# Optimization experiments

Measured on AMD Instinct MI355X. Metric: run time of the kernel, lower is better.

Reference implementation:

```python
import jax, jax.numpy as jnp
import numpy as np

B, N, D_IN, D_OUT = 4, 2048, 1024, 1024

def setup_inputs() -> dict:
    key = jax.random.key(0)
    ks = jax.random.split(key, 7)
    s_in = 1.0 / np.sqrt(D_IN)
    return {
        "X": jax.random.normal(ks[0], (B, N, D_IN), dtype=jnp.float32),
        "Wq": jax.random.uniform(ks[1], (D_IN, D_OUT), jnp.float32, -s_in, s_in),
        "bq": jax.random.uniform(ks[2], (D_OUT,), jnp.float32, -s_in, s_in),
        "Wk": jax.random.uniform(ks[3], (D_IN, D_OUT), jnp.float32, -s_in, s_in),
        "bk": jax.random.uniform(ks[4], (D_OUT,), jnp.float32, -s_in, s_in),
        "Wv": jax.random.uniform(ks[5], (D_IN, D_OUT), jnp.float32, -s_in, s_in),
        "bv": jax.random.uniform(ks[6], (D_OUT,), jnp.float32, -s_in, s_in),
    }

def reference(X, Wq, bq, Wk, bk, Wv, bv):
    # QKV projections: [B,N,D_in] @ [D_in,D_out] -> [B,N,D_out]
    q = jnp.einsum('bnd,de->bne', X, Wq) + bq
    k = jnp.einsum('bnd,de->bne', X, Wk) + bk
    v = jnp.einsum('bnd,de->bne', X, Wv) + bv
    # Unscaled attention (faithful: original has no 1/sqrt(d))
    scores = jnp.einsum('bne,bme->bnm', q, k)  # [B,N,N]
    weights = jax.nn.softmax(scores, axis=-1)
    return jnp.einsum('bnm,bme->bne', weights, v)
```

## Files before the change

kernel.cpp:

```cpp
#include <hip/hip_runtime.h>
#include <hip/hip_bf16.h>
#include <hip/hip_fp16.h>
#include <stdint.h>
#include <math.h>


typedef unsigned short ushort_t;
typedef __attribute__((ext_vector_type(8))) _Float16  f16x8;
typedef __attribute__((ext_vector_type(4))) _Float16  f16x4;
typedef __attribute__((ext_vector_type(4))) float     f32x4;

__device__ __forceinline__ void async_load16(const void* g, void* l) {
  __builtin_amdgcn_global_load_lds(
      (const __attribute__((address_space(1))) void*)g,
      (__attribute__((address_space(3))) void*)l, 16, 0, 0);
}

#define BARR do { __builtin_amdgcn_sched_barrier(0); \
                  __builtin_amdgcn_s_barrier();      \
                  __builtin_amdgcn_sched_barrier(0); } while (0)

#define A0OFF 0
#define B0OFF 16384
#define A1OFF 32768
#define B1OFF 49152

template<int SHIFT>
__device__ __forceinline__ void stage_half(const ushort_t* __restrict__ gb,
                                           int k0, int q, ushort_t* lt, int t)
{
#pragma unroll
  for (int j = 0; j < 2; ++j) {
    const int i   = j * 64 + (t >> 3);
    const int row = ((i >> SHIFT) << (SHIFT + 1)) | (q << SHIFT) | (i & ((1 << SHIFT) - 1));
    const int ch  = (t & 7) ^ (row & 7);
    async_load16(gb + (long)row * 1024 + k0 + ch * 8, lt + row * 64 + (t & 7) * 8);
  }
}

#define RD_A(TP, QM)                                                          \
  do { _Pragma("unroll") for (int m_ = 0; m_ < 4; ++m_) {                     \
    af[m_][0] = *(const f16x8*)&(TP)[(arow0 + (QM)*64 + m_*16) * 64 + ck0];   \
    af[m_][1] = *(const f16x8*)&(TP)[(arow0 + (QM)*64 + m_*16) * 64 + ck1];   \
  } } while (0)

#define RD_B(TP, QN)                                                          \
  do { _Pragma("unroll") for (int n_ = 0; n_ < 2; ++n_) {                     \
    bf[n_][0] = *(const f16x8*)&(TP)[(brow0 + (QN)*32 + n_*16) * 64 + ck0];   \
    bf[n_][1] = *(const f16x8*)&(TP)[(brow0 + (QN)*32 + n_*16) * 64 + ck1];   \
  } } while (0)

#define MM(QM, QN)                                                            \
  do { __builtin_amdgcn_s_setprio(1);                                         \
  _Pragma("unroll") for (int kh_ = 0; kh_ < 2; ++kh_)                         \
    _Pragma("unroll") for (int m_ = 0; m_ < 4; ++m_)                          \
      _Pragma("unroll") for (int n_ = 0; n_ < 2; ++n_)                        \
        acc[(QM)*4+m_][(QN)*2+n_] = __builtin_amdgcn_mfma_f32_16x16x32_f16(   \
            af[m_][kh_], bf[n_][kh_], acc[(QM)*4+m_][(QN)*2+n_], 0, 0, 0);    \
  __builtin_amdgcn_s_setprio(0); } while (0)

template<bool LAST>
__device__ __forceinline__ void iter256(const ushort_t* __restrict__ Ab,
                                        const ushort_t* __restrict__ Bb,
                                        ushort_t* lds, f32x4 (&acc)[8][4],
                                        int ka, int t, int arow0, int brow0,
                                        int ck0, int ck1)
{
  const int kb = ka + 64, kc = ka + 128, kd = ka + 192;
  f16x8 af[4][2], bf[2][2];

  RD_A(lds + A0OFF, 0); RD_B(lds + B0OFF, 0);
  stage_half<5>(Bb, kb, 0, lds + B1OFF, t);
  BARR; MM(0, 0); BARR;

  RD_B(lds + B0OFF, 1);
  if constexpr (!LAST) stage_half<6>(Ab, kc, 0, lds + A0OFF, t);
  BARR; MM(0, 1); BARR;

  RD_A(lds + A0OFF, 1);
  if constexpr (!LAST) stage_half<5>(Bb, kc, 1, lds + B0OFF, t);
  BARR; MM(1, 1); BARR;

  RD_B(lds + B0OFF, 0);
  if constexpr (!LAST) stage_half<6>(Ab, kc, 1, lds + A0OFF, t);
  BARR; MM(1, 0);
  if constexpr (LAST) asm volatile("s_waitcnt vmcnt(0)" ::: "memory");
  else                asm volatile("s_waitcnt vmcnt(6)" ::: "memory");
  BARR;

  RD_A(lds + A1OFF, 0); RD_B(lds + B1OFF, 0);
  if constexpr (!LAST) stage_half<5>(Bb, kc, 0, lds + B0OFF, t);
  BARR; MM(0, 0); BARR;

  RD_B(lds + B1OFF, 1);
  if constexpr (!LAST) stage_half<6>(Ab, kd, 0, lds + A1OFF, t);
  BARR; MM(0, 1); BARR;

  RD_A(lds + A1OFF, 1);
  if constexpr (!LAST) stage_half<5>(Bb, kd, 1, lds + B1OFF, t);
  BARR; MM(1, 1); BARR;

  RD_B(lds + B1OFF, 0);
  if constexpr (!LAST) stage_half<6>(Ab, kd, 1, lds + A1OFF, t);
  BARR; MM(1, 0);
  if constexpr (!LAST) asm volatile("s_waitcnt vmcnt(6)" ::: "memory");
  BARR;
}

__device__ __forceinline__ void gemm256(const ushort_t* __restrict__ Ab,
                                        const ushort_t* __restrict__ Bb,
                                        ushort_t* lds, f32x4 (&acc)[8][4])
{
  const int t    = threadIdx.x;
  const int lane = t & 63;
  const int wave = t >> 6;
  const int wr   = wave >> 2;
  const int wc   = wave & 3;
  const int arow0 = wr * 128 + (lane & 15);
  const int brow0 = wc * 64  + (lane & 15);
  const int ck0 = (((lane >> 4)    ) ^ (lane & 7)) * 8;
  const int ck1 = ((4 + (lane >> 4)) ^ (lane & 7)) * 8;

  stage_half<6>(Ab,  0, 0, lds + A0OFF, t);
  stage_half<5>(Bb,  0, 1, lds + B0OFF, t);
  stage_half<6>(Ab,  0, 1, lds + A0OFF, t);
  stage_half<5>(Bb,  0, 0, lds + B0OFF, t);
  stage_half<6>(Ab, 64, 0, lds + A1OFF, t);
  stage_half<5>(Bb, 64, 1, lds + B1OFF, t);
  stage_half<6>(Ab, 64, 1, lds + A1OFF, t);
  asm volatile("s_waitcnt vmcnt(6)" ::: "memory");
  BARR;

#pragma unroll 1
  for (int it = 0; it < 7; ++it)
    iter256<false>(Ab, Bb, lds, acc, it * 128, t, arow0, brow0, ck0, ck1);
  iter256<true>(Ab, Bb, lds, acc, 896, t, arow0, brow0, ck0, ck1);
}

#define NA0 0
#define NB0 16384
#define NA1 24576
#define NB1 40960

__device__ __forceinline__ void stage_A_n(const ushort_t* __restrict__ gb, long ldk,
                                          int k0, int q, ushort_t* lt, int t)
{
#pragma unroll
  for (int j = 0; j < 2; ++j) {
    const int i   = j * 64 + (t >> 3);
    const int row = ((i >> 5) << 6) | (q << 5) | (i & 31);
    const int ch  = (t & 7) ^ (row & 7);
    async_load16(gb + (long)row * ldk + k0 + ch * 8, lt + row * 64 + (t & 7) * 8);
  }
}

__device__ __forceinline__ void stage_B_n(const ushort_t* __restrict__ gb, long ldk,
                                          int k0, int q, ushort_t* lt, int t)
{
  const int i   = t >> 3;
  const int row = ((i >> 5) << 6) | (q << 5) | (i & 31);
  const int ch  = (t & 7) ^ (row & 7);
  async_load16(gb + (long)row * ldk + k0 + ch * 8, lt + row * 64 + (t & 7) * 8);
}

#define RDN_A(TP, QM)                                                         \
  do { _Pragma("unroll") for (int m_ = 0; m_ < 2; ++m_) {                     \
    af[m_][0] = *(const f16x8*)&(TP)[(arow_l + (QM)*32 + m_*16) * 64 + ck0];  \
    af[m_][1] = *(const f16x8*)&(TP)[(arow_l + (QM)*32 + m_*16) * 64 + ck1];  \
  } } while (0)

#define RDN_AS(TP, QM, S)                                                     \
  do { _Pragma("unroll") for (int m_ = 0; m_ < 2; ++m_) {                     \
    af[m_][0] = *(const f16x8*)&(TP)[(arow_l + (QM)*32 + m_*16) * 64 + ck0] * (S)[(QM)*2+m_]; \
    af[m_][1] = *(const f16x8*)&(TP)[(arow_l + (QM)*32 + m_*16) * 64 + ck1] * (S)[(QM)*2+m_]; \
  } } while (0)

#define RDN_B2(TP, QN, BF)                                                    \
  do { _Pragma("unroll") for (int n_ = 0; n_ < 2; ++n_) {                     \
    (BF)[n_][0] = *(const f16x8*)&(TP)[(brow_l + (QN)*32 + n_*16) * 64 + ck0];\
    (BF)[n_][1] = *(const f16x8*)&(TP)[(brow_l + (QN)*32 + n_*16) * 64 + ck1];\
  } } while (0)

#define MM2(QM)                                                               \
  do { __builtin_amdgcn_s_setprio(1);                                         \
  _Pragma("unroll") for (int kh_ = 0; kh_ < 2; ++kh_)                         \
    _Pragma("unroll") for (int m_ = 0; m_ < 2; ++m_)                          \
      _Pragma("unroll") for (int n_ = 0; n_ < 2; ++n_) {                      \
        acc[(QM)*2+m_][n_]   = __builtin_amdgcn_mfma_f32_16x16x32_f16(        \
            af[m_][kh_], bq0[n_][kh_], acc[(QM)*2+m_][n_], 0, 0, 0);          \
        acc[(QM)*2+m_][2+n_] = __builtin_amdgcn_mfma_f32_16x16x32_f16(        \
            af[m_][kh_], bq1[n_][kh_], acc[(QM)*2+m_][2+n_], 0, 0, 0);        \
      }                                                                       \
  __builtin_amdgcn_s_setprio(0); } while (0)

template<bool LAST>
__device__ __forceinline__ void iter4_n(const ushort_t* __restrict__ Ab,
                                        const ushort_t* __restrict__ Bb,
                                        long lda, long ldb,
                                        ushort_t* lds, f32x4 (&acc)[4][4],
                                        int ka, int t, int arow_l, int brow_l,
                                        int ck0, int ck1)
{
  const int kb = ka + 64, kc = ka + 128, kd = ka + 192;
  f16x8 af[2][2], bq0[2][2], bq1[2][2];

  RDN_A(lds + NA0, 0);
  RDN_B2(lds + NB0, 0, bq0);
  RDN_B2(lds + NB0, 1, bq1);
  stage_B_n(Bb, ldb, kb, 1, lds + NB1, t);
  stage_A_n(Ab, lda, kb, 1, lds + NA1, t);
  BARR; MM2(0); BARR;

  RDN_A(lds + NA0, 1);
  if constexpr (!LAST) {
    stage_A_n(Ab, lda, kc, 0, lds + NA0, t);
    stage_B_n(Bb, ldb, kc, 0, lds + NB0, t);
  }
  BARR; MM2(1);
  if constexpr (LAST) asm volatile("s_waitcnt vmcnt(0)" ::: "memory");
  else                asm volatile("s_waitcnt vmcnt(3)" ::: "memory");
  BARR;

  RDN_A(lds + NA1, 0);
  RDN_B2(lds + NB1, 0, bq0);
  RDN_B2(lds + NB1, 1, bq1);
  if constexpr (!LAST) {
    stage_B_n(Bb, ldb, kc, 1, lds + NB0, t);
    stage_A_n(Ab, lda, kc, 1, lds + NA0, t);
  }
  BARR; MM2(0); BARR;

  RDN_A(lds + NA1, 1);
  if constexpr (!LAST) {
    stage_A_n(Ab, lda, kd, 0, lds + NA1, t);
    stage_B_n(Bb, ldb, kd, 0, lds + NB1, t);
  }
  BARR; MM2(1);
  if constexpr (!LAST) asm volatile("s_waitcnt vmcnt(3)" ::: "memory");
  BARR;
}

template<bool LAST>
__device__ __forceinline__ void pv_iter4(const ushort_t* __restrict__ Ab,
                                         const ushort_t* __restrict__ Bb,
                                         ushort_t* lds, const float (*ScL)[256],
                                         f32x4 (&acc)[4][4],
                                         int ka, int t, int arow_l, int brow_l,
                                         int ck0, int ck1)
{
  const int kb = ka + 64, kc = ka + 128, kd = ka + 192;
  const int cba = ka >> 6;
  f16x8 af[2][2], bq0[2][2], bq1[2][2];
  _Float16 sa[4], sb[4];
#pragma unroll
  for (int s = 0; s < 4; ++s) {
    sa[s] = (_Float16)ScL[cba][arow_l + s * 16];
    sb[s] = (_Float16)ScL[cba + 1][arow_l + s * 16];
  }

  RDN_AS(lds + NA0, 0, sa);
  RDN_B2(lds + NB0, 0, bq0);
  RDN_B2(lds + NB0, 1, bq1);
  stage_B_n(Bb, 2048, kb, 1, lds + NB1, t);
  stage_A_n(Ab, 2048, kb, 1, lds + NA1, t);
  BARR; MM2(0); BARR;

  RDN_AS(lds + NA0, 1, sa);
  if constexpr (!LAST) {
    stage_A_n(Ab, 2048, kc, 0, lds + NA0, t);
    stage_B_n(Bb, 2048, kc, 0, lds + NB0, t);
  }
  BARR; MM2(1);
  if constexpr (LAST) asm volatile("s_waitcnt vmcnt(0)" ::: "memory");
  else                asm volatile("s_waitcnt vmcnt(3)" ::: "memory");
  BARR;

  RDN_AS(lds + NA1, 0, sb);
  RDN_B2(lds + NB1, 0, bq0);
  RDN_B2(lds + NB1, 1, bq1);
  if constexpr (!LAST) {
    stage_B_n(Bb, 2048, kc, 1, lds + NB0, t);
    stage_A_n(Ab, 2048, kc, 1, lds + NA0, t);
  }
  BARR; MM2(0); BARR;

  RDN_AS(lds + NA1, 1, sb);
  if constexpr (!LAST) {
    stage_A_n(Ab, 2048, kd, 0, lds + NA1, t);
    stage_B_n(Bb, 2048, kd, 0, lds + NB1, t);
  }
  BARR; MM2(1);
  if constexpr (!LAST) asm volatile("s_waitcnt vmcnt(3)" ::: "memory");
  BARR;
}

#define PROLOGUE4(LDA, LDB)                                 \
  do {                                                      \
    stage_A_n(Ab, (LDA),  0, 0, lds + NA0, t);              \
    stage_B_n(Bb, (LDB),  0, 0, lds + NB0, t);              \
    stage_B_n(Bb, (LDB),  0, 1, lds + NB0, t);              \
    stage_A_n(Ab, (LDA),  0, 1, lds + NA0, t);              \
    stage_A_n(Ab, (LDA), 64, 0, lds + NA1, t);              \
    stage_B_n(Bb, (LDB), 64, 0, lds + NB1, t);              \
    asm volatile("s_waitcnt vmcnt(3)" ::: "memory");        \
    BARR;                                                   \
  } while (0)

__global__ __launch_bounds__(512, 2)
void qkv4_kernel(const ushort_t* __restrict__ A, const ushort_t* __restrict__ BT,
                 const float* __restrict__ bq, const float* __restrict__ bk,
                 const float* __restrict__ bvp,
                 __half* __restrict__ Qh, __half* __restrict__ Kh,
                 ushort_t* __restrict__ Vt)
{
  __shared__ __align__(16) ushort_t lds[49152];

  const int nb = gridDim.x * gridDim.y;
  int id = blockIdx.y * gridDim.x + blockIdx.x;
  id = (id & 7) * (nb >> 3) + (id >> 3);
  const int bx = id % gridDim.x;
  const int by = id / gridDim.x;

  const ushort_t* Ab = A  + (long)by * 256 * 1024;
  const ushort_t* Bb = BT + (long)bx * 128 * 1024;

  const int t    = threadIdx.x;
  const int lane = t & 63;
  const int wave = t >> 6;
  const int wr   = wave >> 1;
  const int wc   = wave & 1;
  const int arow_l = wr * 64 + (lane & 15);
  const int brow_l = wc * 64 + (lane & 15);
  const int ck0 = (((lane >> 4)    ) ^ (lane & 7)) * 8;
  const int ck1 = ((4 + (lane >> 4)) ^ (lane & 7)) * 8;

  f32x4 acc[4][4];
  const f32x4 zero = {0.0f, 0.0f, 0.0f, 0.0f};
#pragma unroll
  for (int i = 0; i < 4; ++i)
#pragma unroll
    for (int j = 0; j < 4; ++j) acc[i][j] = zero;

  PROLOGUE4(1024, 1024);
#pragma unroll 1
  for (int it = 0; it < 7; ++it)
    iter4_n<false>(Ab, Bb, 1024, 1024, lds, acc, it * 128, t, arow_l, brow_l, ck0, ck1);
  iter4_n<true>(Ab, Bb, 1024, 1024, lds, acc, 896, t, arow_l, brow_l, ck0, ck1);

  const int er = (lane >> 4) * 4, ec = lane & 15;
  const int tgt = bx >> 3;
  const float* bias = (tgt == 0) ? bq : (tgt == 1) ? bk : bvp;

#pragma unroll
  for (int ni = 0; ni < 4; ++ni) {
    const int col = (bx & 7) * 128 + wc * 64 + ni * 16 + ec;
    const float bval = bias[col];
#pragma unroll
    for (int mi = 0; mi < 4; ++mi) {
      const long grow0 = (long)by * 256 + wr * 64 + mi * 16 + er;
      if (tgt < 2) {
        __half* o = (tgt == 0) ? Qh : Kh;
#pragma unroll
        for (int r = 0; r < 4; ++r)
          o[(grow0 + r) * 1024 + col] = __float2half(acc[mi][ni][r] + bval);
      } else {
        const long b  = grow0 >> 11;
        const long ml = grow0 & 2047;
        f16x4 v4;
#pragma unroll
        for (int r = 0; r < 4; ++r) v4[r] = (_Float16)(acc[mi][ni][r] + bval);
        *(f16x4*)&Vt[b * 2097152 + (long)col * 2048 + ml] = v4;
      }
    }
  }
}

__global__ __launch_bounds__(512, 2)
void qk256_kernel(const ushort_t* __restrict__ Q, const ushort_t* __restrict__ Kh,
                  __half* __restrict__ S, float* __restrict__ PM, float* __restrict__ PS)
{
  __shared__ __align__(16) ushort_t lds[65536];

  const int nb = gridDim.x * gridDim.y;
  int id = blockIdx.y * gridDim.x + blockIdx.x;
  id = (id & 7) * (nb >> 3) + (id >> 3);
  const int bx = id % gridDim.x;
  const int by = id / gridDim.x;
  const long z = blockIdx.z;

  const ushort_t* Ab = Q  + z * 2048 * 1024 + (long)by * 256 * 1024;
  const ushort_t* Bb = Kh + z * 2048 * 1024 + (long)bx * 256 * 1024;
  __half* Sb = S + z * 2048 * 2048;

  f32x4 acc[8][4];
  const f32x4 zero = {0.0f, 0.0f, 0.0f, 0.0f};
#pragma unroll
  for (int i = 0; i < 8; ++i)
#pragma unroll
    for (int j = 0; j < 4; ++j) acc[i][j] = zero;

  gemm256(Ab, Bb, lds, acc);

  const int t = threadIdx.x, lane = t & 63, wave = t >> 6;
  const int wr = wave >> 2, wc = wave & 3;
  const int er = (lane >> 4) * 4, ec = lane & 15;
  const int cc = bx * 4 + wc;
  float* PMb = PM + z * 32 * 2048 + (long)cc * 2048;
  float* PSb = PS + z * 32 * 2048 + (long)cc * 2048;

#pragma unroll
  for (int m8 = 0; m8 < 8; ++m8)
#pragma unroll
    for (int r = 0; r < 4; ++r) {
      float m = fmaxf(fmaxf(acc[m8][0][r], acc[m8][1][r]),
                      fmaxf(acc[m8][2][r], acc[m8][3][r]));
      m = fmaxf(m, __shfl_xor(m, 1));
      m = fmaxf(m, __shfl_xor(m, 2));
      m = fmaxf(m, __shfl_xor(m, 4));
      m = fmaxf(m, __shfl_xor(m, 8));
      float s = 0.0f;
#pragma unroll
      for (int n4 = 0; n4 < 4; ++n4) {
        const float e = __expf(acc[m8][n4][r] - m);
        acc[m8][n4][r] = e;
        s += e;
      }
      s += __shfl_xor(s, 1);
      s += __shfl_xor(s, 2);
      s += __shfl_xor(s, 4);
      s += __shfl_xor(s, 8);
      if (ec == 0) {
        const long row = (long)by * 256 + wr * 128 + m8 * 16 + er + r;
        PMb[row] = m;
        PSb[row] = s;
      }
    }

#pragma unroll
  for (int n4 = 0; n4 < 4; ++n4) {
    const long col = (long)bx * 256 + wc * 64 + n4 * 16 + ec;
#pragma unroll
    for (int m8 = 0; m8 < 8; ++m8)
#pragma unroll
      for (int r = 0; r < 4; ++r) {
        const long grow = (long)by * 256 + wr * 128 + m8 * 16 + er + r;
        Sb[grow * 2048 + col] = __float2half(acc[m8][n4][r]);
      }
  }
}

__global__ __launch_bounds__(512, 2)
void pv4_kernel(const ushort_t* __restrict__ S, const ushort_t* __restrict__ Vt,
                const float* __restrict__ PM, const float* __restrict__ PS,
                float* __restrict__ Out)
{
  __shared__ __align__(16) ushort_t lds[49152];
  __shared__ float ScL[32][256];

  const int nb = gridDim.x * gridDim.y;
  int id = blockIdx.y * gridDim.x + blockIdx.x;
  id = (id & 7) * (nb >> 3) + (id >> 3);
  const int bx = id % gridDim.x;
  const int by = id / gridDim.x;
  const long z = blockIdx.z;

  const ushort_t* Ab = S  + z * 4194304 + (long)by * 256 * 2048;
  const ushort_t* Bb = Vt + z * 2097152 + (long)bx * 128 * 2048;
  float* Cb = Out + z * 2048 * 1024;

  const int t = threadIdx.x;

  if (t < 256) {
    const long row = (long)by * 256 + t;
    const float* PMb = PM + z * 32 * 2048;
    const float* PSb = PS + z * 32 * 2048;
    float pm[32];
    float m = -3.4e38f;
#pragma unroll
    for (int cb = 0; cb < 32; ++cb) {
      pm[cb] = PMb[(long)cb * 2048 + row];
      m = fmaxf(m, pm[cb]);
    }
    float l = 0.0f;
#pragma unroll
    for (int cb = 0; cb < 32; ++cb)
      l += PSb[(long)cb * 2048 + row] * __expf(pm[cb] - m);
    const float inv = 1.0f / l;
#pragma unroll
    for (int cb = 0; cb < 32; ++cb)
      ScL[cb][t] = __expf(pm[cb] - m) * inv;
  }
  __syncthreads();

  const int lane = t & 63;
  const int wave = t >> 6;
  const int wr   = wave >> 1;
  const int wc   = wave & 1;
  const int arow_l = wr * 64 + (lane & 15);
  const int brow_l = wc * 64 + (lane & 15);
  const int ck0 = (((lane >> 4)    ) ^ (lane & 7)) * 8;
  const int ck1 = ((4 + (lane >> 4)) ^ (lane & 7)) * 8;

  f32x4 acc[4][4];
  const f32x4 zero = {0.0f, 0.0f, 0.0f, 0.0f};
#pragma unroll
  for (int i = 0; i < 4; ++i)
#pragma unroll
    for (int j = 0; j < 4; ++j) acc[i][j] = zero;

  PROLOGUE4(2048, 2048);
#pragma unroll 1
  for (int it = 0; it < 15; ++it)
    pv_iter4<false>(Ab, Bb, lds, ScL, acc, it * 128, t, arow_l, brow_l, ck0, ck1);
  pv_iter4<true>(Ab, Bb, lds, ScL, acc, 1920, t, arow_l, brow_l, ck0, ck1);

  const int er = (lane >> 4) * 4, ec = lane & 15;
#pragma unroll
  for (int ni = 0; ni < 4; ++ni) {
    const int gcol = bx * 128 + wc * 64 + ni * 16 + ec;
#pragma unroll
    for (int mi = 0; mi < 4; ++mi) {
#pragma unroll
      for (int r = 0; r < 4; ++r) {
        const long grow = (long)by * 256 + wr * 64 + mi * 16 + er + r;
        Cb[grow * 1024 + gcol] = acc[mi][ni][r];
      }
    }
  }
}

__global__ __launch_bounds__(256)
void prep_kernel(const float* __restrict__ W0, const float* __restrict__ W1,
                 const float* __restrict__ W2, __half* __restrict__ dstW,
                 const float* __restrict__ X, __half* __restrict__ Xh)
{
  __shared__ float tile[32][33];
  const int z = blockIdx.z;
  if (z < 3) {
    const float* src = (z == 0) ? W0 : (z == 1) ? W1 : W2;
    __half* d = dstW + (long)z * 1024 * 1024;
    const int c0 = blockIdx.x * 32;
    const int r0 = blockIdx.y * 32;
    const int tx = threadIdx.x & 31;
    const int ty = threadIdx.x >> 5;
#pragma unroll
    for (int i = 0; i < 32; i += 8)
      tile[ty + i][tx] = src[(long)(r0 + ty + i) * 1024 + (c0 + tx)];
    __syncthreads();
#pragma unroll
    for (int i = 0; i < 32; i += 8)
      d[(long)(c0 + ty + i) * 1024 + (r0 + tx)] = __float2half(tile[tx][ty + i]);
  } else {
    const int bid = blockIdx.y * gridDim.x + blockIdx.x;
    const long i = (((long)(z - 3) * 1024 + bid) * 256 + threadIdx.x) * 8;
    const float4 a = *(const float4*)(X + i);
    const float4 b = *(const float4*)(X + i + 4);
    f16x8 h;
    h[0] = (_Float16)a.x; h[1] = (_Float16)a.y; h[2] = (_Float16)a.z; h[3] = (_Float16)a.w;
    h[4] = (_Float16)b.x; h[5] = (_Float16)b.y; h[6] = (_Float16)b.z; h[7] = (_Float16)b.w;
    *(f16x8*)((ushort_t*)Xh + i) = h;
  }
}

__global__ __launch_bounds__(256)
void cvt_f32_f16_kernel(const float* __restrict__ src, __half* __restrict__ dst, long n)
{
  const long i = ((long)blockIdx.x * 256 + threadIdx.x) * 8;
  if (i + 8 > n) return;
  const float4 a = *(const float4*)(src + i);
  const float4 b = *(const float4*)(src + i + 4);
  f16x8 h;
  h[0] = (_Float16)a.x; h[1] = (_Float16)a.y; h[2] = (_Float16)a.z; h[3] = (_Float16)a.w;
  h[4] = (_Float16)b.x; h[5] = (_Float16)b.y; h[6] = (_Float16)b.z; h[7] = (_Float16)b.w;
  *(f16x8*)((ushort_t*)dst + i) = h;
}

__global__ __launch_bounds__(256)
void transpose_cvt3_kernel(const float* __restrict__ W0, const float* __restrict__ W1,
                           const float* __restrict__ W2, __half* __restrict__ dst)
{
  __shared__ float tile[32][33];
  const int z = blockIdx.z;
  const float* src = (z == 0) ? W0 : (z == 1) ? W1 : W2;
  __half* d = dst + (long)z * 1024 * 1024;
  const int c0 = blockIdx.x * 32;
  const int r0 = blockIdx.y * 32;
  const int tx = threadIdx.x & 31;
  const int ty = threadIdx.x >> 5;
#pragma unroll
  for (int i = 0; i < 32; i += 8)
    tile[ty + i][tx] = src[(long)(r0 + ty + i) * 1024 + (c0 + tx)];
  __syncthreads();
#pragma unroll
  for (int i = 0; i < 32; i += 8)
    d[(long)(c0 + ty + i) * 1024 + (r0 + tx)] = __float2half(tile[tx][ty + i]);
}

extern "C" void kernel_launch(void* const* d_in, const int* in_sizes, int n_in,
                              void* d_out, int out_size, void* d_ws, size_t ws_size,
                              hipStream_t stream)
{
  const int  Bb = 4, Nn = 2048, Dd = 1024;
  const long BN = (long)Bb * Nn;

  const float* X  = (const float*)d_in[0];
  const float* Wq = (const float*)d_in[1];
  const float* bq = (const float*)d_in[2];
  const float* Wk = (const float*)d_in[3];
  const float* bk = (const float*)d_in[4];
  const float* Wv = (const float*)d_in[5];
  const float* bv = (const float*)d_in[6];
  float* Out      = (float*)d_out;

  uint8_t* w = (uint8_t*)d_ws;
  ushort_t* Wt = (ushort_t*)w;  w += (size_t)3 * Dd * Dd * 2;

  const size_t statsBytes = (size_t)Bb * 32 * Nn * 4;
  const size_t fullNeed = (size_t)3 * Dd * Dd * 2
                        + 4 * ((size_t)BN * Dd * 2)
                        + (size_t)Bb * Nn * Nn * 2
                        + 2 * statsBytes;

  if (ws_size >= fullNeed) {
    ushort_t* Xh = (ushort_t*)w;  w += (size_t)BN * Dd * 2;
    ushort_t* Q  = (ushort_t*)w;  w += (size_t)BN * Dd * 2;
    ushort_t* Kb = (ushort_t*)w;  w += (size_t)BN * Dd * 2;
    ushort_t* Vt = (ushort_t*)w;  w += (size_t)BN * Dd * 2;
    ushort_t* S  = (ushort_t*)w;  w += (size_t)Bb * Nn * Nn * 2;
    float*    PM = (float*)w;     w += statsBytes;
    float*    PS = (float*)w;

    prep_kernel<<<dim3(32, 32, 7), 256, 0, stream>>>(Wq, Wk, Wv, (__half*)Wt, X, (__half*)Xh);

    qkv4_kernel<<<dim3(3 * Dd / 128, BN / 256, 1), 512, 0, stream>>>(
        Xh, Wt, bq, bk, bv, (__half*)Q, (__half*)Kb, Vt);

    qk256_kernel<<<dim3(Nn / 256, Nn / 256, Bb), 512, 0, stream>>>(
        Q, Kb, (__half*)S, PM, PS);

    pv4_kernel<<<dim3(Dd / 128, Nn / 256, Bb), 512, 0, stream>>>(
        S, Vt, PM, PS, Out);
  } else {
    ushort_t* Xh = (ushort_t*)w;  w += (size_t)Nn * Dd * 2;
    ushort_t* Q  = (ushort_t*)w;  w += (size_t)Nn * Dd * 2;
    ushort_t* Kb = (ushort_t*)w;  w += (size_t)Nn * Dd * 2;
    ushort_t* Vt = (ushort_t*)w;  w += (size_t)Nn * Dd * 2;
    ushort_t* S  = (ushort_t*)w;  w += (size_t)Nn * Nn * 2;
    float*    PM = (float*)w;     w += (size_t)32 * Nn * 4;
    float*    PS = (float*)w;

    transpose_cvt3_kernel<<<dim3(Dd / 32, Dd / 32, 3), 256, 0, stream>>>(Wq, Wk, Wv, (__half*)Wt);

    for (int b = 0; b < Bb; ++b) {
      const float* Xb = X + (long)b * Nn * Dd;
      cvt_f32_f16_kernel<<<dim3((unsigned)((long)Nn * Dd / (8 * 256))), 256, 0, stream>>>(
          Xb, (__half*)Xh, (long)Nn * Dd);
      qkv4_kernel<<<dim3(3 * Dd / 128, Nn / 256, 1), 512, 0, stream>>>(
          Xh, Wt, bq, bk, bv, (__half*)Q, (__half*)Kb, Vt);
      qk256_kernel<<<dim3(Nn / 256, Nn / 256, 1), 512, 0, stream>>>(
          Q, Kb, (__half*)S, PM, PS);
      pv4_kernel<<<dim3(Dd / 128, Nn / 256, 1), 512, 0, stream>>>(
          S, Vt, PM, PS, Out + (long)b * Nn * Dd);
    }
  }
}
```

Baseline: 261.1 us.

## Register double-buffer LDS fragments and shrink QK tile to 256x128

Replaces the three GEMM main loops with a register-prefetch pipeline: A/B fragments for the next sub-step are read from LDS into a second register set while MFMAs run on the current set. In the PV kernel the per-row softmax scale is now applied at MFMA time rather than at fragment load. The QK kernel moves from 256x256 tiles to the 256x128 tile shape shared with the other kernels, doubling its grid and the number of partial max/sum stat columns per row (still 32). The aim is to hide LDS read latency behind matrix math and raise occupancy, at the cost of more VGPR pressure and a longer prologue.

```diff
diff --git a/kernel.cpp b/kernel.cpp
--- a/kernel.cpp
+++ b/kernel.cpp
@@ -20,123 +20,6 @@
                   __builtin_amdgcn_s_barrier();      \
                   __builtin_amdgcn_sched_barrier(0); } while (0)
 
-#define A0OFF 0
-#define B0OFF 16384
-#define A1OFF 32768
-#define B1OFF 49152
-
-template<int SHIFT>
-__device__ __forceinline__ void stage_half(const ushort_t* __restrict__ gb,
-                                           int k0, int q, ushort_t* lt, int t)
-{
-#pragma unroll
-  for (int j = 0; j < 2; ++j) {
-    const int i   = j * 64 + (t >> 3);
-    const int row = ((i >> SHIFT) << (SHIFT + 1)) | (q << SHIFT) | (i & ((1 << SHIFT) - 1));
-    const int ch  = (t & 7) ^ (row & 7);
-    async_load16(gb + (long)row * 1024 + k0 + ch * 8, lt + row * 64 + (t & 7) * 8);
-  }
-}
-
-#define RD_A(TP, QM)                                                          \
-  do { _Pragma("unroll") for (int m_ = 0; m_ < 4; ++m_) {                     \
-    af[m_][0] = *(const f16x8*)&(TP)[(arow0 + (QM)*64 + m_*16) * 64 + ck0];   \
-    af[m_][1] = *(const f16x8*)&(TP)[(arow0 + (QM)*64 + m_*16) * 64 + ck1];   \
-  } } while (0)
-
-#define RD_B(TP, QN)                                                          \
-  do { _Pragma("unroll") for (int n_ = 0; n_ < 2; ++n_) {                     \
-    bf[n_][0] = *(const f16x8*)&(TP)[(brow0 + (QN)*32 + n_*16) * 64 + ck0];   \
-    bf[n_][1] = *(const f16x8*)&(TP)[(brow0 + (QN)*32 + n_*16) * 64 + ck1];   \
-  } } while (0)
-
-#define MM(QM, QN)                                                            \
-  do { __builtin_amdgcn_s_setprio(1);                                         \
-  _Pragma("unroll") for (int kh_ = 0; kh_ < 2; ++kh_)                         \
-    _Pragma("unroll") for (int m_ = 0; m_ < 4; ++m_)                          \
-      _Pragma("unroll") for (int n_ = 0; n_ < 2; ++n_)                        \
-        acc[(QM)*4+m_][(QN)*2+n_] = __builtin_amdgcn_mfma_f32_16x16x32_f16(   \
-            af[m_][kh_], bf[n_][kh_], acc[(QM)*4+m_][(QN)*2+n_], 0, 0, 0);    \
-  __builtin_amdgcn_s_setprio(0); } while (0)
-
-template<bool LAST>
-__device__ __forceinline__ void iter256(const ushort_t* __restrict__ Ab,
-                                        const ushort_t* __restrict__ Bb,
-                                        ushort_t* lds, f32x4 (&acc)[8][4],
-                                        int ka, int t, int arow0, int brow0,
-                                        int ck0, int ck1)
-{
-  const int kb = ka + 64, kc = ka + 128, kd = ka + 192;
-  f16x8 af[4][2], bf[2][2];
-
-  RD_A(lds + A0OFF, 0); RD_B(lds + B0OFF, 0);
-  stage_half<5>(Bb, kb, 0, lds + B1OFF, t);
-  BARR; MM(0, 0); BARR;
-
-  RD_B(lds + B0OFF, 1);
-  if constexpr (!LAST) stage_half<6>(Ab, kc, 0, lds + A0OFF, t);
-  BARR; MM(0, 1); BARR;
-
-  RD_A(lds + A0OFF, 1);
-  if constexpr (!LAST) stage_half<5>(Bb, kc, 1, lds + B0OFF, t);
-  BARR; MM(1, 1); BARR;
-
-  RD_B(lds + B0OFF, 0);
-  if constexpr (!LAST) stage_half<6>(Ab, kc, 1, lds + A0OFF, t);
-  BARR; MM(1, 0);
-  if constexpr (LAST) asm volatile("s_waitcnt vmcnt(0)" ::: "memory");
-  else                asm volatile("s_waitcnt vmcnt(6)" ::: "memory");
-  BARR;
-
-  RD_A(lds + A1OFF, 0); RD_B(lds + B1OFF, 0);
-  if constexpr (!LAST) stage_half<5>(Bb, kc, 0, lds + B0OFF, t);
-  BARR; MM(0, 0); BARR;
-
-  RD_B(lds + B1OFF, 1);
-  if constexpr (!LAST) stage_half<6>(Ab, kd, 0, lds + A1OFF, t);
-  BARR; MM(0, 1); BARR;
-
-  RD_A(lds + A1OFF, 1);
-  if constexpr (!LAST) stage_half<5>(Bb, kd, 1, lds + B1OFF, t);
-  BARR; MM(1, 1); BARR;
-
-  RD_B(lds + B1OFF, 0);
-  if constexpr (!LAST) stage_half<6>(Ab, kd, 1, lds + A1OFF, t);
-  BARR; MM(1, 0);
-  if constexpr (!LAST) asm volatile("s_waitcnt vmcnt(6)" ::: "memory");
-  BARR;
-}
-
-__device__ __forceinline__ void gemm256(const ushort_t* __restrict__ Ab,
-                                        const ushort_t* __restrict__ Bb,
-                                        ushort_t* lds, f32x4 (&acc)[8][4])
-{
-  const int t    = threadIdx.x;
-  const int lane = t & 63;
-  const int wave = t >> 6;
-  const int wr   = wave >> 2;
-  const int wc   = wave & 3;
-  const int arow0 = wr * 128 + (lane & 15);
-  const int brow0 = wc * 64  + (lane & 15);
-  const int ck0 = (((lane >> 4)    ) ^ (lane & 7)) * 8;
-  const int ck1 = ((4 + (lane >> 4)) ^ (lane & 7)) * 8;
-
-  stage_half<6>(Ab,  0, 0, lds + A0OFF, t);
-  stage_half<5>(Bb,  0, 1, lds + B0OFF, t);
-  stage_half<6>(Ab,  0, 1, lds + A0OFF, t);
-  stage_half<5>(Bb,  0, 0, lds + B0OFF, t);
-  stage_half<6>(Ab, 64, 0, lds + A1OFF, t);
-  stage_half<5>(Bb, 64, 1, lds + B1OFF, t);
-  stage_half<6>(Ab, 64, 1, lds + A1OFF, t);
-  asm volatile("s_waitcnt vmcnt(6)" ::: "memory");
-  BARR;
-
-#pragma unroll 1
-  for (int it = 0; it < 7; ++it)
-    iter256<false>(Ab, Bb, lds, acc, it * 128, t, arow0, brow0, ck0, ck1);
-  iter256<true>(Ab, Bb, lds, acc, 896, t, arow0, brow0, ck0, ck1);
-}
-
 #define NA0 0
 #define NB0 16384
 #define NA1 24576
@@ -163,155 +46,164 @@
   async_load16(gb + (long)row * ldk + k0 + ch * 8, lt + row * 64 + (t & 7) * 8);
 }
 
-#define RDN_A(TP, QM)                                                         \
+#define RD_A4(SET, BASE, QM)                                                  \
   do { _Pragma("unroll") for (int m_ = 0; m_ < 2; ++m_) {                     \
-    af[m_][0] = *(const f16x8*)&(TP)[(arow_l + (QM)*32 + m_*16) * 64 + ck0];  \
-    af[m_][1] = *(const f16x8*)&(TP)[(arow_l + (QM)*32 + m_*16) * 64 + ck1];  \
+    SET[m_][0] = *(const f16x8*)&lds[(BASE) + (arow_l + (QM)*32 + m_*16) * 64 + ck0]; \
+    SET[m_][1] = *(const f16x8*)&lds[(BASE) + (arow_l + (QM)*32 + m_*16) * 64 + ck1]; \
   } } while (0)
 
-#define RDN_AS(TP, QM, S)                                                     \
-  do { _Pragma("unroll") for (int m_ = 0; m_ < 2; ++m_) {                     \
-    af[m_][0] = *(const f16x8*)&(TP)[(arow_l + (QM)*32 + m_*16) * 64 + ck0] * (S)[(QM)*2+m_]; \
-    af[m_][1] = *(const f16x8*)&(TP)[(arow_l + (QM)*32 + m_*16) * 64 + ck1] * (S)[(QM)*2+m_]; \
-  } } while (0)
-
-#define RDN_B2(TP, QN, BF)                                                    \
-  do { _Pragma("unroll") for (int n_ = 0; n_ < 2; ++n_) {                     \
-    (BF)[n_][0] = *(const f16x8*)&(TP)[(brow_l + (QN)*32 + n_*16) * 64 + ck0];\
-    (BF)[n_][1] = *(const f16x8*)&(TP)[(brow_l + (QN)*32 + n_*16) * 64 + ck1];\
-  } } while (0)
-
-#define MM2(QM)                                                               \
+#define RD_B4(SET, BASE)                                                      \
+  do { _Pragma("unroll") for (int q_ = 0; q_ < 2; ++q_)                       \
+    _Pragma("unroll") for (int n_ = 0; n_ < 2; ++n_) {                        \
+      SET[q_][n_][0] = *(const f16x8*)&lds[(BASE) + (brow_l + q_*32 + n_*16) * 64 + ck0]; \
+      SET[q_][n_][1] = *(const f16x8*)&lds[(BASE) + (brow_l + q_*32 + n_*16) * 64 + ck1]; \
+    } } while (0)
+
+#define MM16(AS, BS, QM)                                                      \
   do { __builtin_amdgcn_s_setprio(1);                                         \
   _Pragma("unroll") for (int kh_ = 0; kh_ < 2; ++kh_)                         \
     _Pragma("unroll") for (int m_ = 0; m_ < 2; ++m_)                          \
       _Pragma("unroll") for (int n_ = 0; n_ < 2; ++n_) {                      \
         acc[(QM)*2+m_][n_]   = __builtin_amdgcn_mfma_f32_16x16x32_f16(        \
-            af[m_][kh_], bq0[n_][kh_], acc[(QM)*2+m_][n_], 0, 0, 0);          \
+            AS[m_][kh_], BS[0][n_][kh_], acc[(QM)*2+m_][n_], 0, 0, 0);        \
         acc[(QM)*2+m_][2+n_] = __builtin_amdgcn_mfma_f32_16x16x32_f16(        \
-            af[m_][kh_], bq1[n_][kh_], acc[(QM)*2+m_][2+n_], 0, 0, 0);        \
+            AS[m_][kh_], BS[1][n_][kh_], acc[(QM)*2+m_][2+n_], 0, 0, 0);      \
       }                                                                       \
   __builtin_amdgcn_s_setprio(0); } while (0)
 
+#define MM16S(AS, BS, QM, SC)                                                 \
+  do { __builtin_amdgcn_s_setprio(1);                                         \
+  _Pragma("unroll") for (int m_ = 0; m_ < 2; ++m_)                            \
+    _Pragma("unroll") for (int kh_ = 0; kh_ < 2; ++kh_) {                     \
+      const f16x8 as_ = AS[m_][kh_] * (_Float16)(SC)[(QM)*2+m_];              \
+      _Pragma("unroll") for (int n_ = 0; n_ < 2; ++n_) {                      \
+        acc[(QM)*2+m_][n_]   = __builtin_amdgcn_mfma_f32_16x16x32_f16(        \
+            as_, BS[0][n_][kh_], acc[(QM)*2+m_][n_], 0, 0, 0);                \
+        acc[(QM)*2+m_][2+n_] = __builtin_amdgcn_mfma_f32_16x16x32_f16(        \
+            as_, BS[1][n_][kh_], acc[(QM)*2+m_][2+n_], 0, 0, 0);              \
+      } }                                                                     \
+  __builtin_amdgcn_s_setprio(0); } while (0)
+
 template<bool LAST>
-__device__ __forceinline__ void iter4_n(const ushort_t* __restrict__ Ab,
-                                        const ushort_t* __restrict__ Bb,
-                                        long lda, long ldb,
-                                        ushort_t* lds, f32x4 (&acc)[4][4],
-                                        int ka, int t, int arow_l, int brow_l,
-                                        int ck0, int ck1)
-{
-  const int kb = ka + 64, kc = ka + 128, kd = ka + 192;
-  f16x8 af[2][2], bq0[2][2], bq1[2][2];
-
-  RDN_A(lds + NA0, 0);
-  RDN_B2(lds + NB0, 0, bq0);
-  RDN_B2(lds + NB0, 1, bq1);
-  stage_B_n(Bb, ldb, kb, 1, lds + NB1, t);
-  stage_A_n(Ab, lda, kb, 1, lds + NA1, t);
-  BARR; MM2(0); BARR;
-
-  RDN_A(lds + NA0, 1);
-  if constexpr (!LAST) {
-    stage_A_n(Ab, lda, kc, 0, lds + NA0, t);
-    stage_B_n(Bb, ldb, kc, 0, lds + NB0, t);
-  }
-  BARR; MM2(1);
+__device__ __forceinline__ void iterRA(const ushort_t* __restrict__ Ab,
+                                       const ushort_t* __restrict__ Bb,
+                                       long lda, long ldb,
+                                       ushort_t* lds, f32x4 (&acc)[4][4],
+                                       int ka, int t, int arow_l, int brow_l,
+                                       int ck0, int ck1,
+                                       f16x8 (&aF)[2][2], f16x8 (&aG)[2][2],
+                                       f16x8 (&bF)[2][2][2], f16x8 (&bG)[2][2][2])
+{
+  const int kc = ka + 128, kd = ka + 192;
+
+  RD_A4(aG, NA0, 1);
+  if constexpr (!LAST) { stage_A_n(Ab, lda, kc, 0, lds + NA0, t);
+                         stage_B_n(Bb, ldb, kc, 0, lds + NB0, t); }
+  BARR;
+  MM16(aF, bF, 0);
   if constexpr (LAST) asm volatile("s_waitcnt vmcnt(0)" ::: "memory");
   else                asm volatile("s_waitcnt vmcnt(3)" ::: "memory");
   BARR;
-
-  RDN_A(lds + NA1, 0);
-  RDN_B2(lds + NB1, 0, bq0);
-  RDN_B2(lds + NB1, 1, bq1);
+  RD_A4(aF, NA1, 0);
+  RD_B4(bG, NB1);
+  if constexpr (!LAST) { stage_A_n(Ab, lda, kc, 1, lds + NA0, t);
+                         stage_B_n(Bb, ldb, kc, 1, lds + NB0, t); }
+  BARR;
+  MM16(aG, bF, 1);
+  BARR;
+  RD_A4(aG, NA1, 1);
+  if constexpr (!LAST) { stage_A_n(Ab, lda, kd, 0, lds + NA1, t);
+                         stage_B_n(Bb, ldb, kd, 0, lds + NB1, t); }
+  BARR;
+  MM16(aF, bG, 0);
+  if constexpr (!LAST) asm volatile("s_waitcnt vmcnt(3)" ::: "memory");
+  BARR;
   if constexpr (!LAST) {
-    stage_B_n(Bb, ldb, kc, 1, lds + NB0, t);
-    stage_A_n(Ab, lda, kc, 1, lds + NA0, t);
-  }
-  BARR; MM2(0); BARR;
-
-  RDN_A(lds + NA1, 1);
-  if constexpr (!LAST) {
-    stage_A_n(Ab, lda, kd, 0, lds + NA1, t);
-    stage_B_n(Bb, ldb, kd, 0, lds + NB1, t);
-  }
-  BARR; MM2(1);
-  if constexpr (!LAST) asm volatile("s_waitcnt vmcnt(3)" ::: "memory");
+    RD_A4(aF, NA0, 0);
+    RD_B4(bF, NB0);
+    stage_A_n(Ab, lda, kd, 1, lds + NA1, t);
+    stage_B_n(Bb, ldb, kd, 1, lds + NB1, t);
+  }
+  BARR;
+  MM16(aG, bG, 1);
   BARR;
 }
 
 template<bool LAST>
-__device__ __forceinline__ void pv_iter4(const ushort_t* __restrict__ Ab,
-                                         const ushort_t* __restrict__ Bb,
-                                         ushort_t* lds, const float (*ScL)[256],
-                                         f32x4 (&acc)[4][4],
-                                         int ka, int t, int arow_l, int brow_l,
-                                         int ck0, int ck1)
-{
-  const int kb = ka + 64, kc = ka + 128, kd = ka + 192;
+__device__ __forceinline__ void pv_iterRA(const ushort_t* __restrict__ Ab,
+                                          const ushort_t* __restrict__ Bb,
+                                          ushort_t* lds, const float (*ScL)[256],
+                                          f32x4 (&acc)[4][4],
+                                          int ka, int t, int arow_l, int brow_l,
+                                          int ck0, int ck1,
+                                          f16x8 (&aF)[2][2], f16x8 (&aG)[2][2],
+                                          f16x8 (&bF)[2][2][2], f16x8 (&bG)[2][2][2])
+{
+  const int kc = ka + 128, kd = ka + 192;
   const int cba = ka >> 6;
-  f16x8 af[2][2], bq0[2][2], bq1[2][2];
-  _Float16 sa[4], sb[4];
+  float sa4[4], sb4[4];
 #pragma unroll
   for (int s = 0; s < 4; ++s) {
-    sa[s] = (_Float16)ScL[cba][arow_l + s * 16];
-    sb[s] = (_Float16)ScL[cba + 1][arow_l + s * 16];
-  }
-
-  RDN_AS(lds + NA0, 0, sa);
-  RDN_B2(lds + NB0, 0, bq0);
-  RDN_B2(lds + NB0, 1, bq1);
-  stage_B_n(Bb, 2048, kb, 1, lds + NB1, t);
-  stage_A_n(Ab, 2048, kb, 1, lds + NA1, t);
-  BARR; MM2(0); BARR;
-
-  RDN_AS(lds + NA0, 1, sa);
-  if constexpr (!LAST) {
-    stage_A_n(Ab, 2048, kc, 0, lds + NA0, t);
-    stage_B_n(Bb, 2048, kc, 0, lds + NB0, t);
-  }
-  BARR; MM2(1);
+    sa4[s] = ScL[cba][arow_l + s * 16];
+    sb4[s] = ScL[cba + 1][arow_l + s * 16];
+  }
+
+  RD_A4(aG, NA0, 1);
+  if constexpr (!LAST) { stage_A_n(Ab, 2048, kc, 0, lds + NA0, t);
+                         stage_B_n(Bb, 2048, kc, 0, lds + NB0, t); }
+  BARR;
+  MM16S(aF, bF, 0, sa4);
   if constexpr (LAST) asm volatile("s_waitcnt vmcnt(0)" ::: "memory");
   else                asm volatile("s_waitcnt vmcnt(3)" ::: "memory");
   BARR;
-
-  RDN_AS(lds + NA1, 0, sb);
-  RDN_B2(lds + NB1, 0, bq0);
-  RDN_B2(lds + NB1, 1, bq1);
+  RD_A4(aF, NA1, 0);
+  RD_B4(bG, NB1);
+  if constexpr (!LAST) { stage_A_n(Ab, 2048, kc, 1, lds + NA0, t);
+                         stage_B_n(Bb, 2048, kc, 1, lds + NB0, t); }
+  BARR;
+  MM16S(aG, bF, 1, sa4);
+  BARR;
+  RD_A4(aG, NA1, 1);
+  if constexpr (!LAST) { stage_A_n(Ab, 2048, kd, 0, lds + NA1, t);
+                         stage_B_n(Bb, 2048, kd, 0, lds + NB1, t); }
+  BARR;
+  MM16S(aF, bG, 0, sb4);
+  if constexpr (!LAST) asm volatile("s_waitcnt vmcnt(3)" ::: "memory");
+  BARR;
   if constexpr (!LAST) {
-    stage_B_n(Bb, 2048, kc, 1, lds + NB0, t);
-    stage_A_n(Ab, 2048, kc, 1, lds + NA0, t);
-  }
-  BARR; MM2(0); BARR;
-
-  RDN_AS(lds + NA1, 1, sb);
-  if constexpr (!LAST) {
-    stage_A_n(Ab, 2048, kd, 0, lds + NA1, t);
-    stage_B_n(Bb, 2048, kd, 0, lds + NB1, t);
-  }
-  BARR; MM2(1);
-  if constexpr (!LAST) asm volatile("s_waitcnt vmcnt(3)" ::: "memory");
-  BARR;
-}
-
-#define PROLOGUE4(LDA, LDB)                                 \
+    RD_A4(aF, NA0, 0);
+    RD_B4(bF, NB0);
+    stage_A_n(Ab, 2048, kd, 1, lds + NA1, t);
+    stage_B_n(Bb, 2048, kd, 1, lds + NB1, t);
+  }
+  BARR;
+  MM16S(aG, bG, 1, sb4);
+  BARR;
+}
+
+#define PROLOGUE_RA(LDA, LDB)                               \
   do {                                                      \
     stage_A_n(Ab, (LDA),  0, 0, lds + NA0, t);              \
     stage_B_n(Bb, (LDB),  0, 0, lds + NB0, t);              \
+    stage_A_n(Ab, (LDA),  0, 1, lds + NA0, t);              \
     stage_B_n(Bb, (LDB),  0, 1, lds + NB0, t);              \
-    stage_A_n(Ab, (LDA),  0, 1, lds + NA0, t);              \
+    asm volatile("s_waitcnt vmcnt(0)" ::: "memory");        \
+    BARR;                                                   \
+    RD_A4(aF, NA0, 0);                                      \
+    RD_B4(bF, NB0);                                         \
     stage_A_n(Ab, (LDA), 64, 0, lds + NA1, t);              \
     stage_B_n(Bb, (LDB), 64, 0, lds + NB1, t);              \
-    asm volatile("s_waitcnt vmcnt(3)" ::: "memory");        \
+    stage_A_n(Ab, (LDA), 64, 1, lds + NA1, t);              \
+    stage_B_n(Bb, (LDB), 64, 1, lds + NB1, t);              \
     BARR;                                                   \
   } while (0)
 
 __global__ __launch_bounds__(512, 2)
-void qkv4_kernel(const ushort_t* __restrict__ A, const ushort_t* __restrict__ BT,
-                 const float* __restrict__ bq, const float* __restrict__ bk,
-                 const float* __restrict__ bvp,
-                 __half* __restrict__ Qh, __half* __restrict__ Kh,
-                 ushort_t* __restrict__ Vt)
+void qkv_ra_kernel(const ushort_t* __restrict__ A, const ushort_t* __restrict__ BT,
+                   const float* __restrict__ bq, const float* __restrict__ bk,
+                   const float* __restrict__ bvp,
+                   __half* __restrict__ Qh, __half* __restrict__ Kh,
+                   ushort_t* __restrict__ Vt)
 {
   __shared__ __align__(16) ushort_t lds[49152];
 
@@ -341,11 +233,15 @@
 #pragma unroll
     for (int j = 0; j < 4; ++j) acc[i][j] = zero;
 
-  PROLOGUE4(1024, 1024);
+  f16x8 aF[2][2], aG[2][2], bF[2][2][2], bG[2][2][2];
+
+  PROLOGUE_RA(1024, 1024);
 #pragma unroll 1
   for (int it = 0; it < 7; ++it)
-    iter4_n<false>(Ab, Bb, 1024, 1024, lds, acc, it * 128, t, arow_l, brow_l, ck0, ck1);
-  iter4_n<true>(Ab, Bb, 1024, 1024, lds, acc, 896, t, arow_l, brow_l, ck0, ck1);
+    iterRA<false>(Ab, Bb, 1024, 1024, lds, acc, it * 128, t, arow_l, brow_l,
+                  ck0, ck1, aF, aG, bF, bG);
+  iterRA<true>(Ab, Bb, 1024, 1024, lds, acc, 896, t, arow_l, brow_l,
+               ck0, ck1, aF, aG, bF, bG);
 
   const int er = (lane >> 4) * 4, ec = lane & 15;
   const int tgt = bx >> 3;
@@ -376,10 +272,10 @@
 }
 
 __global__ __launch_bounds__(512, 2)
-void qk256_kernel(const ushort_t* __restrict__ Q, const ushort_t* __restrict__ Kh,
+void qk_ra_kernel(const ushort_t* __restrict__ Q, const ushort_t* __restrict__ Kh,
                   __half* __restrict__ S, float* __restrict__ PM, float* __restrict__ PS)
 {
-  __shared__ __align__(16) ushort_t lds[65536];
+  __shared__ __align__(16) ushort_t lds[49152];
 
   const int nb = gridDim.x * gridDim.y;
   int id = blockIdx.y * gridDim.x + blockIdx.x;
@@ -389,109 +285,10 @@
   const long z = blockIdx.z;
 
   const ushort_t* Ab = Q  + z * 2048 * 1024 + (long)by * 256 * 1024;
-  const ushort_t* Bb = Kh + z * 2048 * 1024 + (long)bx * 256 * 1024;
+  const ushort_t* Bb = Kh + z * 2048 * 1024 + (long)bx * 128 * 1024;
   __half* Sb = S + z * 2048 * 2048;
 
-  f32x4 acc[8][4];
-  const f32x4 zero = {0.0f, 0.0f, 0.0f, 0.0f};
-#pragma unroll
-  for (int i = 0; i < 8; ++i)
-#pragma unroll
-    for (int j = 0; j < 4; ++j) acc[i][j] = zero;
-
-  gemm256(Ab, Bb, lds, acc);
-
-  const int t = threadIdx.x, lane = t & 63, wave = t >> 6;
-  const int wr = wave >> 2, wc = wave & 3;
-  const int er = (lane >> 4) * 4, ec = lane & 15;
-  const int cc = bx * 4 + wc;
-  float* PMb = PM + z * 32 * 2048 + (long)cc * 2048;
-  float* PSb = PS + z * 32 * 2048 + (long)cc * 2048;
-
-#pragma unroll
-  for (int m8 = 0; m8 < 8; ++m8)
-#pragma unroll
-    for (int r = 0; r < 4; ++r) {
-      float m = fmaxf(fmaxf(acc[m8][0][r], acc[m8][1][r]),
-                      fmaxf(acc[m8][2][r], acc[m8][3][r]));
-      m = fmaxf(m, __shfl_xor(m, 1));
-      m = fmaxf(m, __shfl_xor(m, 2));
-      m = fmaxf(m, __shfl_xor(m, 4));
-      m = fmaxf(m, __shfl_xor(m, 8));
-      float s = 0.0f;
-#pragma unroll
-      for (int n4 = 0; n4 < 4; ++n4) {
-        const float e = __expf(acc[m8][n4][r] - m);
-        acc[m8][n4][r] = e;
-        s += e;
-      }
-      s += __shfl_xor(s, 1);
-      s += __shfl_xor(s, 2);
-      s += __shfl_xor(s, 4);
-      s += __shfl_xor(s, 8);
-      if (ec == 0) {
-        const long row = (long)by * 256 + wr * 128 + m8 * 16 + er + r;
-        PMb[row] = m;
-        PSb[row] = s;
-      }
-    }
-
-#pragma unroll
-  for (int n4 = 0; n4 < 4; ++n4) {
-    const long col = (long)bx * 256 + wc * 64 + n4 * 16 + ec;
-#pragma unroll
-    for (int m8 = 0; m8 < 8; ++m8)
-#pragma unroll
-      for (int r = 0; r < 4; ++r) {
-        const long grow = (long)by * 256 + wr * 128 + m8 * 16 + er + r;
-        Sb[grow * 2048 + col] = __float2half(acc[m8][n4][r]);
-      }
-  }
-}
-
-__global__ __launch_bounds__(512, 2)
-void pv4_kernel(const ushort_t* __restrict__ S, const ushort_t* __restrict__ Vt,
-                const float* __restrict__ PM, const float* __restrict__ PS,
-                float* __restrict__ Out)
-{
-  __shared__ __align__(16) ushort_t lds[49152];
-  __shared__ float ScL[32][256];
-
-  const int nb = gridDim.x * gridDim.y;
-  int id = blockIdx.y * gridDim.x + blockIdx.x;
-  id = (id & 7) * (nb >> 3) + (id >> 3);
-  const int bx = id % gridDim.x;
-  const int by = id / gridDim.x;
-  const long z = blockIdx.z;
-
-  const ushort_t* Ab = S  + z * 4194304 + (long)by * 256 * 2048;
-  const ushort_t* Bb = Vt + z * 2097152 + (long)bx * 128 * 2048;
-  float* Cb = Out + z * 2048 * 1024;
-
-  const int t = threadIdx.x;
-
-  if (t < 256) {
-    const long row = (long)by * 256 + t;
-    const float* PMb = PM + z * 32 * 2048;
-    const float* PSb = PS + z * 32 * 2048;
-    float pm[32];
-    float m = -3.4e38f;
-#pragma unroll
-    for (int cb = 0; cb < 32; ++cb) {
-      pm[cb] = PMb[(long)cb * 2048 + row];
-      m = fmaxf(m, pm[cb]);
-    }
-    float l = 0.0f;
-#pragma unroll
-    for (int cb = 0; cb < 32; ++cb)
-      l += PSb[(long)cb * 2048 + row] * __expf(pm[cb] - m);
-    const float inv = 1.0f / l;
-#pragma unroll
-    for (int cb = 0; cb < 32; ++cb)
-      ScL[cb][t] = __expf(pm[cb] - m) * inv;
-  }
-  __syncthreads();
-
+  const int t    = threadIdx.x;
   const int lane = t & 63;
   const int wave = t >> 6;
   const int wr   = wave >> 1;
@@ -508,11 +305,130 @@
 #pragma unroll
     for (int j = 0; j < 4; ++j) acc[i][j] = zero;
 
-  PROLOGUE4(2048, 2048);
+  f16x8 aF[2][2], aG[2][2], bF[2][2][2], bG[2][2][2];
+
+  PROLOGUE_RA(1024, 1024);
+#pragma unroll 1
+  for (int it = 0; it < 7; ++it)
+    iterRA<false>(Ab, Bb, 1024, 1024, lds, acc, it * 128, t, arow_l, brow_l,
+                  ck0, ck1, aF, aG, bF, bG);
+  iterRA<true>(Ab, Bb, 1024, 1024, lds, acc, 896, t, arow_l, brow_l,
+               ck0, ck1, aF, aG, bF, bG);
+
+  const int er = (lane >> 4) * 4, ec = lane & 15;
+  const int cc = bx * 2 + wc;
+  float* PMb = PM + z * 32 * 2048 + (long)cc * 2048;
+  float* PSb = PS + z * 32 * 2048 + (long)cc * 2048;
+
+#pragma unroll
+  for (int mi = 0; mi < 4; ++mi)
+#pragma unroll
+    for (int r = 0; r < 4; ++r) {
+      float m = fmaxf(fmaxf(acc[mi][0][r], acc[mi][1][r]),
+                      fmaxf(acc[mi][2][r], acc[mi][3][r]));
+      m = fmaxf(m, __shfl_xor(m, 1));
+      m = fmaxf(m, __shfl_xor(m, 2));
+      m = fmaxf(m, __shfl_xor(m, 4));
+      m = fmaxf(m, __shfl_xor(m, 8));
+      float s = 0.0f;
+#pragma unroll
+      for (int ni = 0; ni < 4; ++ni) {
+        const float e = __expf(acc[mi][ni][r] - m);
+        acc[mi][ni][r] = e;
+        s += e;
+      }
+      s += __shfl_xor(s, 1);
+      s += __shfl_xor(s, 2);
+      s += __shfl_xor(s, 4);
+      s += __shfl_xor(s, 8);
+      if (ec == 0) {
+        const long row = (long)by * 256 + wr * 64 + mi * 16 + er + r;
+        PMb[row] = m;
+        PSb[row] = s;
+      }
+    }
+
+#pragma unroll
+  for (int ni = 0; ni < 4; ++ni) {
+    const long col = (long)bx * 128 + wc * 64 + ni * 16 + ec;
+#pragma unroll
+    for (int mi = 0; mi < 4; ++mi)
+#pragma unroll
+      for (int r = 0; r < 4; ++r) {
+        const long grow = (long)by * 256 + wr * 64 + mi * 16 + er + r;
+        Sb[grow * 2048 + col] = __float2half(acc[mi][ni][r]);
+      }
+  }
+}
+
+__global__ __launch_bounds__(512, 2)
+void pv_ra_kernel(const ushort_t* __restrict__ S, const ushort_t* __restrict__ Vt,
+                  const float* __restrict__ PM, const float* __restrict__ PS,
+                  float* __restrict__ Out)
+{
+  __shared__ __align__(16) ushort_t lds[49152];
+  __shared__ float ScL[32][256];
+
+  const int nb = gridDim.x * gridDim.y;
+  int id = blockIdx.y * gridDim.x + blockIdx.x;
+  id = (id & 7) * (nb >> 3) + (id >> 3);
+  const int bx = id % gridDim.x;
+  const int by = id / gridDim.x;
+  const long z = blockIdx.z;
+
+  const ushort_t* Ab = S  + z * 4194304 + (long)by * 256 * 2048;
+  const ushort_t* Bb = Vt + z * 2097152 + (long)bx * 128 * 2048;
+  float* Cb = Out + z * 2048 * 1024;
+
+  const int t = threadIdx.x;
+
+  if (t < 256) {
+    const long row = (long)by * 256 + t;
+    const float* PMb = PM + z * 32 * 2048;
+    const float* PSb = PS + z * 32 * 2048;
+    float pm[32];
+    float m = -3.4e38f;
+#pragma unroll
+    for (int cb = 0; cb < 32; ++cb) {
+      pm[cb] = PMb[(long)cb * 2048 + row];
+      m = fmaxf(m, pm[cb]);
+    }
+    float l = 0.0f;
+#pragma unroll
+    for (int cb = 0; cb < 32; ++cb)
+      l += PSb[(long)cb * 2048 + row] * __expf(pm[cb] - m);
+    const float inv = 1.0f / l;
+#pragma unroll
+    for (int cb = 0; cb < 32; ++cb)
+      ScL[cb][t] = __expf(pm[cb] - m) * inv;
+  }
+  __syncthreads();
+
+  const int lane = t & 63;
+  const int wave = t >> 6;
+  const int wr   = wave >> 1;
+  const int wc   = wave & 1;
+  const int arow_l = wr * 64 + (lane & 15);
+  const int brow_l = wc * 64 + (lane & 15);
+  const int ck0 = (((lane >> 4)    ) ^ (lane & 7)) * 8;
+  const int ck1 = ((4 + (lane >> 4)) ^ (lane & 7)) * 8;
+
+  f32x4 acc[4][4];
+  const f32x4 zero = {0.0f, 0.0f, 0.0f, 0.0f};
+#pragma unroll
+  for (int i = 0; i < 4; ++i)
+#pragma unroll
+    for (int j = 0; j < 4; ++j) acc[i][j] = zero;
+
+  f16x8 aF[2][2], aG[2][2], bF[2][2][2], bG[2][2][2];
+
+  PROLOGUE_RA(2048, 2048);
 #pragma unroll 1
   for (int it = 0; it < 15; ++it)
-    pv_iter4<false>(Ab, Bb, lds, ScL, acc, it * 128, t, arow_l, brow_l, ck0, ck1);
-  pv_iter4<true>(Ab, Bb, lds, ScL, acc, 1920, t, arow_l, brow_l, ck0, ck1);
+    pv_iterRA<false>(Ab, Bb, lds, ScL, acc, it * 128, t, arow_l, brow_l,
+                     ck0, ck1, aF, aG, bF, bG);
+  pv_iterRA<true>(Ab, Bb, lds, ScL, acc, 1920, t, arow_l, brow_l,
+                  ck0, ck1, aF, aG, bF, bG);
 
   const int er = (lane >> 4) * 4, ec = lane & 15;
 #pragma unroll
@@ -632,13 +548,13 @@
 
     prep_kernel<<<dim3(32, 32, 7), 256, 0, stream>>>(Wq, Wk, Wv, (__half*)Wt, X, (__half*)Xh);
 
-    qkv4_kernel<<<dim3(3 * Dd / 128, BN / 256, 1), 512, 0, stream>>>(
+    qkv_ra_kernel<<<dim3(3 * Dd / 128, BN / 256, 1), 512, 0, stream>>>(
         Xh, Wt, bq, bk, bv, (__half*)Q, (__half*)Kb, Vt);
 
-    qk256_kernel<<<dim3(Nn / 256, Nn / 256, Bb), 512, 0, stream>>>(
+    qk_ra_kernel<<<dim3(Nn / 128, Nn / 256, Bb), 512, 0, stream>>>(
         Q, Kb, (__half*)S, PM, PS);
 
-    pv4_kernel<<<dim3(Dd / 128, Nn / 256, Bb), 512, 0, stream>>>(
+    pv_ra_kernel<<<dim3(Dd / 128, Nn / 256, Bb), 512, 0, stream>>>(
         S, Vt, PM, PS, Out);
   } else {
     ushort_t* Xh = (ushort_t*)w;  w += (size_t)Nn * Dd * 2;
@@ -655,11 +571,11 @@
       const float* Xb = X + (long)b * Nn * Dd;
       cvt_f32_f16_kernel<<<dim3((unsigned)((long)Nn * Dd / (8 * 256))), 256, 0, stream>>>(
           Xb, (__half*)Xh, (long)Nn * Dd);
-      qkv4_kernel<<<dim3(3 * Dd / 128, Nn / 256, 1), 512, 0, stream>>>(
+      qkv_ra_kernel<<<dim3(3 * Dd / 128, Nn / 256, 1), 512, 0, stream>>>(
           Xh, Wt, bq, bk, bv, (__half*)Q, (__half*)Kb, Vt);
-      qk256_kernel<<<dim3(Nn / 256, Nn / 256, 1), 512, 0, stream>>>(
+      qk_ra_kernel<<<dim3(Nn / 128, Nn / 256, 1), 512, 0, stream>>>(
           Q, Kb, (__half*)S, PM, PS);
-      pv4_kernel<<<dim3(Dd / 128, Nn / 256, 1), 512, 0, stream>>>(
+      pv_ra_kernel<<<dim3(Dd / 128, Nn / 256, 1), 512, 0, stream>>>(
           S, Vt, PM, PS, Out + (long)b * Nn * Dd);
     }
   }
```

Result: faster. 245.3 us (-6.1%).
